# Optimization experiments

Measured on AMD Instinct MI355X. Metric: run time of the kernel, lower is better.

The kernel has to match this reference:

```python
import jax, jax.numpy as jnp
import numpy as np

P_DROP = 0.6  # dropout prob from the source module
N_NODES = 50000
N_EDGES = 800000


def _cheb_edge_weights(edge_index, num_nodes):
    # ChebConv with sym normalization and default lambda_max=2.0:
    # scaled Laplacian hat(L) = 2L/lambda_max - I = -D^{-1/2} A D^{-1/2}
    # (diagonal becomes 0), so edge weight = -1/sqrt(deg[row]*deg[col]).
    row, col = edge_index[0], edge_index[1]
    deg = jnp.zeros((num_nodes,), jnp.float32).at[row].add(1.0)
    dis = jnp.where(deg > 0, jax.lax.rsqrt(jnp.maximum(deg, 1.0)), 0.0)
    return -dis[row] * dis[col]


def _prop(x, row, col, w, n):
    # hat(L) @ x via gather-scale-scatter over the edge list
    return jnp.zeros((n, x.shape[1]), x.dtype).at[row].add(w[:, None] * x[col])


def _cheb_conv(x, row, col, w, W, b, n):
    # Chebyshev recursion: Tx0 = x, Tx1 = hat(L) x, Tx_k = 2 hat(L) Tx_{k-1} - Tx_{k-2}
    Tx0 = x
    out = Tx0 @ W[0]
    Tx1 = _prop(Tx0, row, col, w, n)
    out = out + Tx1 @ W[1]
    for k in range(2, W.shape[0]):
        Tx2 = 2.0 * _prop(Tx1, row, col, w, n) - Tx0
        out = out + Tx2 @ W[k]
        Tx0, Tx1 = Tx1, Tx2
    return out + b


def _dropout(x, key, p):
    keep = jax.random.bernoulli(key, 1.0 - p, x.shape)
    return jnp.where(keep, x * (1.0 / (1.0 - p)), 0.0)


def setup_inputs() -> dict:
    key = jax.random.key(0)
    ks = jax.random.split(key, 8)
    x = jax.random.normal(ks[0], (N_NODES, 64), jnp.float32)
    edge_index = jax.random.randint(ks[1], (2, N_EDGES), 0, N_NODES, jnp.int64)
    W0 = jax.random.normal(ks[2], (2, 64, 64), jnp.float32) * 0.1
    b0 = jnp.zeros((64,), jnp.float32)
    W1 = jax.random.normal(ks[3], (2, 64, 64), jnp.float32) * 0.1
    b1 = jnp.zeros((64,), jnp.float32)
    W2 = jax.random.normal(ks[4], (2, 64, 32), jnp.float32) * 0.1
    b2 = jnp.zeros((32,), jnp.float32)
    return {"x": x, "edge_index": edge_index, "W0": W0, "b0": b0,
            "W1": W1, "b1": b1, "W2": W2, "b2": b2}


def reference(x, edge_index, W0, b0, W1, b1, W2, b2):
    row, col = edge_index[0], edge_index[1]
    n = x.shape[0]
    w = _cheb_edge_weights(edge_index, n)
    dkey = jax.random.key(1)
    params = [(W0, b0), (W1, b1), (W2, b2)]
    for i, (W, b) in enumerate(params):
        x = _dropout(x, jax.random.fold_in(dkey, i), P_DROP)
        x = _cheb_conv(x, row, col, w, W, b, n)
        if i < len(params) - 1:
            x = jax.nn.relu(x)
    return x
```

## Files before the change

kernel.cpp:

```cpp
#include <hip/hip_runtime.h>
#include <stdint.h>

typedef _Float16 half8 __attribute__((ext_vector_type(8)));
typedef float float4v __attribute__((ext_vector_type(4)));

__host__ __device__ inline void tf2x32(uint32_t k0, uint32_t k1,
                                       uint32_t x0, uint32_t x1,
                                       uint32_t* o0, uint32_t* o1) {
  const uint32_t ks2 = k0 ^ k1 ^ 0x1BD11BDAu;
#define ROTL(v, s) (((v) << (s)) | ((v) >> (32 - (s))))
#define RND(r) do { x0 += x1; x1 = ROTL(x1, r); x1 ^= x0; } while (0)
  x0 += k0; x1 += k1;
  RND(13); RND(15); RND(26); RND(6);
  x0 += k1; x1 += ks2 + 1u;
  RND(17); RND(29); RND(16); RND(24);
  x0 += ks2; x1 += k0 + 2u;
  RND(13); RND(15); RND(26); RND(6);
  x0 += k0; x1 += k1 + 3u;
  RND(17); RND(29); RND(16); RND(24);
  x0 += k1; x1 += ks2 + 4u;
  RND(13); RND(15); RND(26); RND(6);
  x0 += ks2; x1 += k0 + 5u;
  *o0 = x0; *o1 = x1;
#undef RND
#undef ROTL
}

__device__ inline bool drop_keep(uint32_t k0, uint32_t k1, uint32_t idx) {
  uint32_t o0, o1;
  tf2x32(k0, k1, 0u, idx, &o0, &o1);
  uint32_t bits = o0 ^ o1;
  float u = __uint_as_float((bits >> 9) | 0x3f800000u) - 1.0f;
  return u < 0.4f;
}

__global__ void k_fill2(const int* __restrict__ row, const int* __restrict__ col,
                        int* __restrict__ cnt, uint16_t* __restrict__ cs,
                        int e, int rows_per_xcd) {
  const int owner = blockIdx.x & 7;
  const int i = (blockIdx.x >> 3) * 256 + threadIdx.x;
  if (i < e) {
    int r = row[i];
    if (r / rows_per_xcd == owner) {
      int pos = atomicAdd(&cnt[r], 1);
      if (pos < 64) cs[(r << 6) + pos] = (uint16_t)col[i];
    }
  }
}

__global__ void k_drop(const float* __restrict__ x, const int* __restrict__ cnt,
                       uint16_t* __restrict__ cs, float* __restrict__ dis,
                       _Float16* __restrict__ y, _Float16* __restrict__ ys,
                       _Float16* __restrict__ ysb, uint32_t k0, uint32_t k1,
                       int n, int nd,
                       const float* __restrict__ W0, const float* __restrict__ W1,
                       const float* __restrict__ W2, _Float16* __restrict__ wh) {
  int i = blockIdx.x * 256 + threadIdx.x;
  if (i < 20480) {
    int d = i;
    if (d < 8192) {
      int o = d >> 7, k = d & 127;
      wh[d] = (_Float16)W0[k * 64 + o];
    } else if (d < 16384) {
      int d1 = d - 8192, o = d1 >> 7, k = d1 & 127;
      wh[d] = (_Float16)W1[k * 64 + o];
    } else {
      int d2 = d - 16384, o = d2 >> 7, k = d2 & 127;
      wh[d] = (_Float16)W2[k * 32 + o];
    }
  }
  if (i < 64) {
    ys[((size_t)n << 6) + i]  = (_Float16)0.f;
    ysb[((size_t)n << 6) + i] = (_Float16)0.f;
  }
  if (i < nd) {
    const int r = i >> 6;
    const int t = i & 63;
    const int d = cnt[r];
    const float dis_r = (d > 0) ? rsqrtf((float)d) : 0.0f;
    float v = drop_keep(k0, k1, (uint32_t)i) ? x[i] * 2.5f : 0.0f;
    y[i]  = (_Float16)v;
    ys[i] = (_Float16)(dis_r * v);
    if (t == 0) dis[r] = dis_r;
    const int cn = d < 64 ? d : 64;
    const int rnd = (cn + 7) & ~7;
    if (t >= cn && t < rnd) cs[(r << 6) + t] = (uint16_t)n;
  }
}

template<int T>
__device__ __forceinline__ void gatherT(int idx_all, int rnd, int g, int sub,
                                        const _Float16* __restrict__ ysg,
                                        uint32_t dummy, float acc[8]) {
  half8 hv[T];
  #pragma unroll
  for (int j = 0; j < T; ++j) {
    int sh = __shfl(idx_all, j * 8 + g, 64);
    uint32_t c = (j * 8 < rnd) ? (uint32_t)(sh & 0xffff) : dummy;
    hv[j] = *(const half8*)((const char*)ysg + (c << 7) + (sub << 4));
  }
  #pragma unroll
  for (int j = 0; j < T; ++j)
    #pragma unroll
    for (int k = 0; k < 8; ++k) acc[k] += (float)hv[j][k];
}

template<int COUT, bool RELU, bool DROPN, bool WBF>
__global__ __launch_bounds__(256, 6) void k_conv(
    const _Float16* __restrict__ yg, const _Float16* __restrict__ ysg,
    const int* __restrict__ cnt, const uint16_t* __restrict__ cs,
    const float* __restrict__ dis, const _Float16* __restrict__ wt,
    const float* __restrict__ b, float* __restrict__ outf,
    _Float16* __restrict__ outb, _Float16* __restrict__ outs,
    uint32_t nk0, uint32_t nk1, int n) {
  constexpr int R  = 16;
  constexpr int TS = 136;
  __shared__ __align__(16) _Float16 xp[R][TS];

  const int wave = threadIdx.x >> 6;
  const int t    = threadIdx.x & 63;
  const int row0 = blockIdx.x * R;
  const int g    = t >> 3;
  const int sub  = t & 7;
  const uint32_t dummy = (uint32_t)n;

  int      idxs[4], ds4[4];
  float    dv4[4];
  _Float16 ygv[4];
  #pragma unroll
  for (int i = 0; i < 4; ++i) {
    int r = row0 + wave * 4 + i;
    r = r < n ? r : n - 1;
    idxs[i] = cs[(r << 6) + t];
    ds4[i]  = cnt[r];
    dv4[i]  = dis[r];
    ygv[i]  = yg[(uint32_t)(r << 6) + t];
  }

  #pragma unroll
  for (int i = 0; i < 4; ++i) {
    const int cn  = ds4[i] < 64 ? ds4[i] : 64;
    const int rnd = (cn + 7) & ~7;
    float acc[8] = {0.f, 0.f, 0.f, 0.f, 0.f, 0.f, 0.f, 0.f};
    if (rnd <= 16)      gatherT<2>(idxs[i], rnd, g, sub, ysg, dummy, acc);
    else if (rnd <= 32) gatherT<4>(idxs[i], rnd, g, sub, ysg, dummy, acc);
    else                gatherT<8>(idxs[i], rnd, g, sub, ysg, dummy, acc);

    const bool b0 = (g & 1), b1 = (g & 2), b2 = (g & 4);
    float a4[4], a2[2], v;
    #pragma unroll
    for (int m = 0; m < 4; ++m) {
      float keep = b0 ? acc[2 * m + 1] : acc[2 * m];
      float send = b0 ? acc[2 * m]     : acc[2 * m + 1];
      a4[m] = keep + __shfl_xor(send, 8, 64);
    }
    #pragma unroll
    for (int m = 0; m < 2; ++m) {
      float keep = b1 ? a4[2 * m + 1] : a4[2 * m];
      float send = b1 ? a4[2 * m]     : a4[2 * m + 1];
      a2[m] = keep + __shfl_xor(send, 16, 64);
    }
    {
      float keep = b2 ? a2[1] : a2[0];
      float send = b2 ? a2[0] : a2[1];
      v = keep + __shfl_xor(send, 32, 64);
    }
    const int rl = wave * 4 + i;
    xp[rl][t]                    = ygv[i];
    xp[rl][64 + (sub * 8 + g)]   = (_Float16)(-dv4[i] * v);
  }
  __syncthreads();

  constexpr int NW = COUT / 16;
  const int nn   = t & 15;
  const int quad = t >> 4;
  if (wave < NW) {
    const int colg = wave * 16 + nn;
    float4v acc = {0.f, 0.f, 0.f, 0.f};
    #pragma unroll
    for (int ks = 0; ks < 4; ++ks) {
      half8 a  = *(const half8*)&xp[nn][quad * 8 + 32 * ks];
      half8 bb = *(const half8*)&wt[(size_t)colg * 128 + quad * 8 + 32 * ks];
      acc = __builtin_amdgcn_mfma_f32_16x16x32_f16(a, bb, acc, 0, 0, 0);
    }
    const float bias = b[colg];
    #pragma unroll
    for (int rg = 0; rg < 4; ++rg) {
      const int rl = quad * 4 + rg;
      const int rr = row0 + rl;
      if (rr < n) {
        float v = acc[rg] + bias;
        if (RELU) v = fmaxf(v, 0.0f);
        if (DROPN) {
          if (drop_keep(nk0, nk1, (uint32_t)(rr * 64 + colg))) v *= 2.5f;
          else v = 0.0f;
        }
        if (WBF) {
          outb[(size_t)rr * COUT + colg] = (_Float16)v;
          outs[(size_t)rr * COUT + colg] = (_Float16)(dis[rr] * v);
        } else {
          outf[(size_t)rr * COUT + colg] = v;
        }
      }
    }
  }
}

extern "C" void kernel_launch(void* const* d_in, const int* in_sizes, int n_in,
                              void* d_out, int out_size, void* d_ws, size_t ws_size,
                              hipStream_t stream) {
  const float* x   = (const float*)d_in[0];
  const int*   ei  = (const int*)d_in[1];
  const float* W0  = (const float*)d_in[2];
  const float* b0  = (const float*)d_in[3];
  const float* W1f = (const float*)d_in[4];
  const float* b1  = (const float*)d_in[5];
  const float* W2  = (const float*)d_in[6];
  const float* b2  = (const float*)d_in[7];
  float* out = (float*)d_out;

  const int n = in_sizes[0] / 64;
  const int e = in_sizes[1] / 2;
  const int* row = ei;
  const int* col = ei + e;

  size_t off = 0;
  auto carve = [&](size_t elems) {
    size_t o = off;
    off += (elems + 255) & ~(size_t)255;
    return o;
  };
  int* base = (int*)d_ws;
  int*      cnt = base + carve(n);
  float*    dis = (float*)(base + carve(n));
  uint16_t* cs  = (uint16_t*)(base + carve((size_t)n * 32));
  _Float16* ya  = (_Float16*)(base + carve((size_t)n * 32));
  _Float16* ysa = (_Float16*)(base + carve((size_t)(n + 1) * 32));
  _Float16* yb  = (_Float16*)(base + carve((size_t)n * 32));
  _Float16* ysb = (_Float16*)(base + carve((size_t)(n + 1) * 32));
  _Float16* wh  = (_Float16*)(base + carve(10240));
  (void)ws_size;
  _Float16* wh0 = wh;
  _Float16* wh1 = wh + 8192;
  _Float16* wh2 = wh + 16384;

  uint32_t dk[3][2];
  for (uint32_t i = 0; i < 3; ++i) tf2x32(0u, 1u, 0u, i, &dk[i][0], &dk[i][1]);

  hipMemsetAsync(cnt, 0, (size_t)n * 4, stream);

  const int nchunk = (e + 255) / 256;
  const int bd = ((n * 64) + 255) / 256;
  const int bc = (n + 15) / 16;
  const int rpx = (n + 7) / 8;

  k_fill2<<<nchunk * 8, 256, 0, stream>>>(row, col, cnt, cs, e, rpx);
  k_drop<<<bd, 256, 0, stream>>>(x, cnt, cs, dis, ya, ysa, ysb,
                                 dk[0][0], dk[0][1], n, n * 64,
                                 W0, W1f, W2, wh);

  k_conv<64, true,  true,  true ><<<bc, 256, 0, stream>>>(
      ya, ysa, cnt, cs, dis, wh0, b0, nullptr, yb, ysb, dk[1][0], dk[1][1], n);
  k_conv<64, true,  true,  true ><<<bc, 256, 0, stream>>>(
      yb, ysb, cnt, cs, dis, wh1, b1, nullptr, ya, ysa, dk[2][0], dk[2][1], n);
  k_conv<32, false, false, false><<<bc, 256, 0, stream>>>(
      ya, ysa, cnt, cs, dis, wh2, b2, out, nullptr, nullptr, 0u, 0u, n);
}
```

Baseline: 189.2 us.

## Assign one node row per wave with 1024-thread blocks in conv kernel

Each conv block now launches 16 waves, and each wave gathers and reduces a single node row instead of four rows per wave across four waves. The 8-slot gather for high-degree rows is split into two 4-slot passes to lower register pressure, and the launch bounds change to match the larger block. The aim is more latency hiding from wave-level parallelism rather than per-wave unrolling. The trade-off is fewer independent loads in flight per wave and a barrier that must now synchronise 16 waves.

```diff
diff --git a/kernel.cpp b/kernel.cpp
--- a/kernel.cpp
+++ b/kernel.cpp
@@ -89,14 +89,15 @@
 }
 
 template<int T>
-__device__ __forceinline__ void gatherT(int idx_all, int rnd, int g, int sub,
+__device__ __forceinline__ void gatherT(int idx_all, int rnd, int jb, int g,
+                                        int sub,
                                         const _Float16* __restrict__ ysg,
                                         uint32_t dummy, float acc[8]) {
   half8 hv[T];
   #pragma unroll
   for (int j = 0; j < T; ++j) {
-    int sh = __shfl(idx_all, j * 8 + g, 64);
-    uint32_t c = (j * 8 < rnd) ? (uint32_t)(sh & 0xffff) : dummy;
+    int sh = __shfl(idx_all, (jb + j) * 8 + g, 64);
+    uint32_t c = ((jb + j) * 8 < rnd) ? (uint32_t)(sh & 0xffff) : dummy;
     hv[j] = *(const half8*)((const char*)ysg + (c << 7) + (sub << 4));
   }
   #pragma unroll
@@ -106,7 +107,7 @@
 }
 
 template<int COUT, bool RELU, bool DROPN, bool WBF>
-__global__ __launch_bounds__(256, 6) void k_conv(
+__global__ __launch_bounds__(1024, 8) void k_conv(
     const _Float16* __restrict__ yg, const _Float16* __restrict__ ysg,
     const int* __restrict__ cnt, const uint16_t* __restrict__ cs,
     const float* __restrict__ dis, const _Float16* __restrict__ wt,
@@ -124,27 +125,25 @@
   const int sub  = t & 7;
   const uint32_t dummy = (uint32_t)n;
 
-  int      idxs[4], ds4[4];
-  float    dv4[4];
-  _Float16 ygv[4];
-  #pragma unroll
-  for (int i = 0; i < 4; ++i) {
-    int r = row0 + wave * 4 + i;
+  {
+    int r = row0 + wave;
     r = r < n ? r : n - 1;
-    idxs[i] = cs[(r << 6) + t];
-    ds4[i]  = cnt[r];
-    dv4[i]  = dis[r];
-    ygv[i]  = yg[(uint32_t)(r << 6) + t];
-  }
-
-  #pragma unroll
-  for (int i = 0; i < 4; ++i) {
-    const int cn  = ds4[i] < 64 ? ds4[i] : 64;
+    const int      idx_all = cs[(r << 6) + t];
+    const int      d       = cnt[r];
+    const float    dv      = dis[r];
+    const _Float16 ygv     = yg[(uint32_t)(r << 6) + t];
+
+    const int cn  = d < 64 ? d : 64;
     const int rnd = (cn + 7) & ~7;
     float acc[8] = {0.f, 0.f, 0.f, 0.f, 0.f, 0.f, 0.f, 0.f};
-    if (rnd <= 16)      gatherT<2>(idxs[i], rnd, g, sub, ysg, dummy, acc);
-    else if (rnd <= 32) gatherT<4>(idxs[i], rnd, g, sub, ysg, dummy, acc);
-    else                gatherT<8>(idxs[i], rnd, g, sub, ysg, dummy, acc);
+    if (rnd <= 16) {
+      gatherT<2>(idx_all, rnd, 0, g, sub, ysg, dummy, acc);
+    } else if (rnd <= 32) {
+      gatherT<4>(idx_all, rnd, 0, g, sub, ysg, dummy, acc);
+    } else {
+      gatherT<4>(idx_all, rnd, 0, g, sub, ysg, dummy, acc);
+      gatherT<4>(idx_all, rnd, 4, g, sub, ysg, dummy, acc);
+    }
 
     const bool b0 = (g & 1), b1 = (g & 2), b2 = (g & 4);
     float a4[4], a2[2], v;
@@ -165,9 +164,8 @@
       float send = b2 ? a2[0] : a2[1];
       v = keep + __shfl_xor(send, 32, 64);
     }
-    const int rl = wave * 4 + i;
-    xp[rl][t]                    = ygv[i];
-    xp[rl][64 + (sub * 8 + g)]   = (_Float16)(-dv4[i] * v);
+    xp[wave][t]                  = ygv;
+    xp[wave][64 + (sub * 8 + g)] = (_Float16)(-dv * v);
   }
   __syncthreads();
 
@@ -259,10 +257,10 @@
                                  dk[0][0], dk[0][1], n, n * 64,
                                  W0, W1f, W2, wh);
 
-  k_conv<64, true,  true,  true ><<<bc, 256, 0, stream>>>(
+  k_conv<64, true,  true,  true ><<<bc, 1024, 0, stream>>>(
       ya, ysa, cnt, cs, dis, wh0, b0, nullptr, yb, ysb, dk[1][0], dk[1][1], n);
-  k_conv<64, true,  true,  true ><<<bc, 256, 0, stream>>>(
+  k_conv<64, true,  true,  true ><<<bc, 1024, 0, stream>>>(
       yb, ysb, cnt, cs, dis, wh1, b1, nullptr, ya, ysa, dk[2][0], dk[2][1], n);
-  k_conv<32, false, false, false><<<bc, 256, 0, stream>>>(
+  k_conv<32, false, false, false><<<bc, 1024, 0, stream>>>(
       ya, ysa, cnt, cs, dis, wh2, b2, out, nullptr, nullptr, 0u, 0u, n);
 }
```

After: 204.4 us. +8.0%, slower.
